# Optimization experiments

Hardware: AMD Instinct MI355X
Metric: run time of the kernel (lower is better)

## Reference

```python
import jax, jax.numpy as jnp
import numpy as np

EPS = 1e-4

def softmax_kernel(data, projection_matrix, is_query):
    # data: [b,h,n,d]; projection_matrix: [m,d]
    d = data.shape[-1]
    m = projection_matrix.shape[0]
    data_normalizer = d ** -0.25
    ratio = m ** -0.5
    # [b,h,n,m]
    data_dash = jnp.einsum('bhnd,md->bhnm', data_normalizer * data, projection_matrix)
    diag_data = jnp.sum(data ** 2, axis=-1, keepdims=True) * 0.5 * data_normalizer ** 2  # [b,h,n,1]
    if is_query:
        stab = jnp.max(data_dash, axis=-1, keepdims=True)
    else:
        stab = jnp.max(data_dash)
    return ratio * (jnp.exp(data_dash - diag_data - stab) + EPS)

def linear_attention(q, k, v):
    # q,k: [b,h,n,m]; v: [b,h,n,e]
    L = k.shape[-2]
    D_inv = 1.0 / jnp.einsum('bhnm,bhm->bhn', q, jnp.mean(k, axis=-2))  # [b,h,n]
    context = jnp.einsum('bhnm,bhne->bhme', k / float(L), v)            # [b,h,m,e]
    out = jnp.einsum('bhnm,bhme->bhne', D_inv[..., None] * q, context)  # [b,h,n,e]
    return out

def setup_inputs() -> dict:
    key = jax.random.key(0)
    k1, k2, k3, k4 = jax.random.split(key, 4)
    b, h, n, d = 4, 8, 4096, 64
    m = 266  # int(d * log(d))
    q = jax.random.normal(k1, (b, h, n, d), dtype=jnp.float32)
    k = jax.random.normal(k2, (b, h, n, d), dtype=jnp.float32)
    v = jax.random.normal(k3, (b, h, n, d), dtype=jnp.float32)
    projection_matrix = jax.random.normal(k4, (m, d), dtype=jnp.float32)
    return {"q": q, "k": k, "v": v, "projection_matrix": projection_matrix}

def reference(q, k, v, projection_matrix):
    qp = softmax_kernel(q, projection_matrix, is_query=True)
    kp = softmax_kernel(k, projection_matrix, is_query=False)
    return linear_attention(qp, kp, v)
```

## Files before the change

kernel.cpp:

```cpp
#include <hip/hip_runtime.h>
#include <cmath>


namespace {
constexpr float NORM       = 0.35355339059327379f;
constexpr float DIAG_SCALE = 0.0625f;
constexpr float EPSV       = 1e-4f;
constexpr float INV_L      = 1.0f / 4096.0f;

constexpr size_t OFF_PT  = 0;
constexpr size_t OFF_U   = OFF_PT + (size_t)64 * 272;
constexpr size_t OFF_u   = OFF_U + (size_t)32 * 272 * 64;
constexpr size_t OFF_SV  = OFF_u + (size_t)32 * 272;
constexpr size_t OFF_SC  = OFF_SV + (size_t)32 * 64;
constexpr size_t OFF_SK  = OFF_SC + (size_t)32 * 64;
constexpr size_t OFF_S   = OFF_SK + 32;
constexpr size_t OFF_CTX = OFF_S + 4;
constexpr size_t WS_FLOATS = OFF_CTX + (size_t)32 * 272 * 68;
}

__device__ __forceinline__ unsigned fenc(float f) {
  unsigned u = __float_as_uint(f);
  return (u & 0x80000000u) ? ~u : (u | 0x80000000u);
}
__device__ __forceinline__ float fdec(unsigned u) {
  return (u & 0x80000000u) ? __uint_as_float(u ^ 0x80000000u) : __uint_as_float(~u);
}

__device__ __forceinline__ void glds4(const float* g, float* l) {
  __builtin_amdgcn_global_load_lds((const __attribute__((address_space(1))) void*)g,
                                   (__attribute__((address_space(3))) void*)l, 4, 0, 0);
}
__device__ __forceinline__ void glds16(const float* g, float* l) {
  __builtin_amdgcn_global_load_lds((const __attribute__((address_space(1))) void*)g,
                                   (__attribute__((address_space(3))) void*)l, 16, 0, 0);
}

__global__ __launch_bounds__(256) void setup_kernel(const float* __restrict__ P,
                                                    float* __restrict__ ws) {
  const int t = threadIdx.x;
  const int elem = blockIdx.x * 256 + t;
  const int td = elem / 272, mm = elem % 272;
  ws[OFF_PT + (size_t)td * 272 + mm] = (mm < 266) ? NORM * P[mm * 64 + td] : 0.0f;
  if (blockIdx.x == 0 && t == 0) ((unsigned*)(ws + OFF_S))[0] = 0x007FFFFFu;
}

#define KQ_ROW(A1R, K4, P0, P1, P2, P3)                                         \
  {                                                                             \
    A1R[0] = fmaf((K4).x, (P0).x, A1R[0]);                                      \
    A1R[1] = fmaf((K4).x, (P0).y, A1R[1]);                                      \
    A1R[2] = fmaf((K4).x, (P0).z, A1R[2]);                                      \
    A1R[3] = fmaf((K4).x, (P0).w, A1R[3]);                                      \
    A1R[0] = fmaf((K4).y, (P1).x, A1R[0]);                                      \
    A1R[1] = fmaf((K4).y, (P1).y, A1R[1]);                                      \
    A1R[2] = fmaf((K4).y, (P1).z, A1R[2]);                                      \
    A1R[3] = fmaf((K4).y, (P1).w, A1R[3]);                                      \
    A1R[0] = fmaf((K4).z, (P2).x, A1R[0]);                                      \
    A1R[1] = fmaf((K4).z, (P2).y, A1R[1]);                                      \
    A1R[2] = fmaf((K4).z, (P2).z, A1R[2]);                                      \
    A1R[3] = fmaf((K4).z, (P2).w, A1R[3]);                                      \
    A1R[0] = fmaf((K4).w, (P3).x, A1R[0]);                                      \
    A1R[1] = fmaf((K4).w, (P3).y, A1R[1]);                                      \
    A1R[2] = fmaf((K4).w, (P3).z, A1R[2]);                                      \
    A1R[3] = fmaf((K4).w, (P3).w, A1R[3]);                                      \
  }

#define QC_ROW(AR, Q4, C0, C1, C2, C3)                                          \
  {                                                                             \
    AR[0] = fmaf((Q4).x, (C0).x, AR[0]);                                        \
    AR[1] = fmaf((Q4).x, (C0).y, AR[1]);                                        \
    AR[2] = fmaf((Q4).x, (C0).z, AR[2]);                                        \
    AR[3] = fmaf((Q4).x, (C0).w, AR[3]);                                        \
    AR[0] = fmaf((Q4).y, (C1).x, AR[0]);                                        \
    AR[1] = fmaf((Q4).y, (C1).y, AR[1]);                                        \
    AR[2] = fmaf((Q4).y, (C1).z, AR[2]);                                        \
    AR[3] = fmaf((Q4).y, (C1).w, AR[3]);                                        \
    AR[0] = fmaf((Q4).z, (C2).x, AR[0]);                                        \
    AR[1] = fmaf((Q4).z, (C2).y, AR[1]);                                        \
    AR[2] = fmaf((Q4).z, (C2).z, AR[2]);                                        \
    AR[3] = fmaf((Q4).z, (C2).w, AR[3]);                                        \
    AR[0] = fmaf((Q4).w, (C3).x, AR[0]);                                        \
    AR[1] = fmaf((Q4).w, (C3).y, AR[1]);                                        \
    AR[2] = fmaf((Q4).w, (C3).z, AR[2]);                                        \
    AR[3] = fmaf((Q4).w, (C3).w, AR[3]);                                        \
  }

__global__ __launch_bounds__(256) void pass_k_fused(const float* __restrict__ kg,
                                                    const float* __restrict__ vg,
                                                    float* __restrict__ ws) {
  __shared__ __align__(16) float pool[12544];
  __shared__ float diagS[64];
  __shared__ float redb[4];

  const int t = threadIdx.x;
  const int mb = blockIdx.x, bh = blockIdx.y, bz = blockIdx.z;
  const int lane = t & 63, wv = t >> 6;

  float* PTs = pool;
  float* kS  = pool + 4096;
  float* vS  = pool + 8448;

  const size_t base = ((size_t)bh * 4096 + (size_t)bz * 1024) * 64;

  if (mb == 4) {
    const int m4 = t & 3, rg1 = t >> 2;
    const int eg = (t >> 2) & 15, rs = t >> 6;

    {
      const int td = t >> 2, m4i = t & 3;
      *(float4*)(PTs + td * 16 + m4i * 4) =
          *(const float4*)(ws + OFF_PT + (size_t)td * 272 + 256 + m4i * 4);
    }

    float acc2[4][4];
#pragma unroll
    for (int i = 0; i < 4; ++i) { acc2[i][0] = acc2[i][1] = acc2[i][2] = acc2[i][3] = 0.f; }
    float uacc[4] = {0, 0, 0, 0};
    float vsum[4] = {0, 0, 0, 0};
    float smax = -INFINITY;

    for (int sc = 0; sc < 16; ++sc) {
      const float* kgp = kg + base + (size_t)sc * 64 * 64;
      const float* vgp = vg + base + (size_t)sc * 64 * 64;
      __syncthreads();
      {
        const int r0 = wv * 16;
#pragma unroll
        for (int r = 0; r < 16; ++r) glds4(kgp + (r0 + r) * 64 + lane, kS + (r0 + r) * 68);
#pragma unroll
        for (int r4 = 0; r4 < 4; ++r4)
          glds16(vgp + (r0 + r4 * 4) * 64 + lane * 4, vS + (r0 + r4 * 4) * 64);
      }
      __syncthreads();
      {
        const int dr = t >> 2, dq = t & 3;
        const float4 s0 = *(const float4*)(kS + dr * 68 + dq * 16);
        const float4 s1 = *(const float4*)(kS + dr * 68 + dq * 16 + 4);
        const float4 s2 = *(const float4*)(kS + dr * 68 + dq * 16 + 8);
        const float4 s3 = *(const float4*)(kS + dr * 68 + dq * 16 + 12);
        float s = s0.x * s0.x;
        s = fmaf(s0.y, s0.y, s); s = fmaf(s0.z, s0.z, s); s = fmaf(s0.w, s0.w, s);
        s = fmaf(s1.x, s1.x, s); s = fmaf(s1.y, s1.y, s); s = fmaf(s1.z, s1.z, s);
        s = fmaf(s1.w, s1.w, s);
        s = fmaf(s2.x, s2.x, s); s = fmaf(s2.y, s2.y, s); s = fmaf(s2.z, s2.z, s);
        s = fmaf(s2.w, s2.w, s);
        s = fmaf(s3.x, s3.x, s); s = fmaf(s3.y, s3.y, s); s = fmaf(s3.z, s3.z, s);
        s = fmaf(s3.w, s3.w, s);
        s += __shfl_xor(s, 1);
        s += __shfl_xor(s, 2);
        if (dq == 0) diagS[dr] = s * DIAG_SCALE;
      }
      __syncthreads();
      float a1[4] = {0, 0, 0, 0};
#pragma unroll
      for (int tb = 0; tb < 16; ++tb) {
        const int td = tb * 4;
        const float4 kv4 = *(const float4*)(kS + rg1 * 68 + td);
        const float4 p0 = *(const float4*)(PTs + (td + 0) * 16 + m4 * 4);
        const float4 p1 = *(const float4*)(PTs + (td + 1) * 16 + m4 * 4);
        const float4 p2 = *(const float4*)(PTs + (td + 2) * 16 + m4 * 4);
        const float4 p3 = *(const float4*)(PTs + (td + 3) * 16 + m4 * 4);
        KQ_ROW(a1, kv4, p0, p1, p2, p3);
      }
      float vals[4];
      {
        const float dg = diagS[rg1];
#pragma unroll
        for (int j = 0; j < 4; ++j) {
          const int m = 256 + m4 * 4 + j;
          float e = 0.f;
          if (m < 266) {
            smax = fmaxf(smax, a1[j]);
            e = __expf(a1[j] - dg);
          }
          vals[j] = e;
        }
      }
      __syncthreads();
      {
        float4 st;
        st.x = vals[0]; st.y = vals[1]; st.z = vals[2]; st.w = vals[3];
        *(float4*)(kS + rg1 * 20 + m4 * 4) = st;
      }
      __syncthreads();
#pragma unroll 2
      for (int nn = 0; nn < 16; ++nn) {
        const int n = rs * 16 + nn;
        const float4 kk4 = *(const float4*)(kS + n * 20 + m4 * 4);
        const float4 vv4 = *(const float4*)(vS + n * 64 + eg * 4);
        const float kk[4] = {kk4.x, kk4.y, kk4.z, kk4.w};
        const float vv[4] = {vv4.x, vv4.y, vv4.z, vv4.w};
#pragma unroll
        for (int i = 0; i < 4; ++i)
#pragma unroll
          for (int j = 0; j < 4; ++j) acc2[i][j] = fmaf(kk[i], vv[j], acc2[i][j]);
        if (eg == 0) {
#pragma unroll
          for (int i = 0; i < 4; ++i) uacc[i] += kk[i];
        }
        if (m4 == 0) {
          vsum[0] += vv[0]; vsum[1] += vv[1]; vsum[2] += vv[2]; vsum[3] += vv[3];
        }
      }
    }
    {
      float* Ub = ws + OFF_U + ((size_t)bh * 272 + 256 + m4 * 4) * 64 + eg * 4;
#pragma unroll
      for (int i = 0; i < 4; ++i)
#pragma unroll
        for (int j = 0; j < 4; ++j) atomicAdd(Ub + (size_t)i * 64 + j, acc2[i][j]);
      if (eg == 0) {
#pragma unroll
        for (int i = 0; i < 4; ++i)
          atomicAdd(ws + OFF_u + (size_t)bh * 272 + 256 + m4 * 4 + i, uacc[i]);
      }
      if (m4 == 0) {
#pragma unroll
        for (int j = 0; j < 4; ++j)
          atomicAdd(ws + OFF_SV + bh * 64 + eg * 4 + j, vsum[j]);
      }
    }
#pragma unroll
    for (int o = 32; o > 0; o >>= 1) smax = fmaxf(smax, __shfl_xor(smax, o));
    if (lane == 0) redb[wv] = smax;
    __syncthreads();
    if (t == 0) {
      const float m = fmaxf(fmaxf(redb[0], redb[1]), fmaxf(redb[2], redb[3]));
      atomicMax((unsigned*)(ws + OFF_S), fenc(m));
    }
    return;
  }

  const int mq = t & 15, rg = t >> 4;
  const int mo = t & 7, eo = (t >> 3) & 7;
  const int rs = t >> 6;

#pragma unroll
  for (int c = 0; c < 4; ++c) {
    const int f4 = c * 256 + t;
    const int td = f4 >> 4, mi = f4 & 15;
    *(float4*)(PTs + td * 64 + mi * 4) =
        *(const float4*)(ws + OFF_PT + (size_t)td * 272 + mb * 64 + mi * 4);
  }

  float acc2[8][8];
#pragma unroll
  for (int i = 0; i < 8; ++i)
#pragma unroll
    for (int j = 0; j < 8; ++j) acc2[i][j] = 0.f;
  float uacc[8] = {0, 0, 0, 0, 0, 0, 0, 0};
  float smax = -INFINITY;

  for (int sc = 0; sc < 16; ++sc) {
    const float* kgp = kg + base + (size_t)sc * 64 * 64;
    const float* vgp = vg + base + (size_t)sc * 64 * 64;
    __syncthreads();
    {
      const int r0 = wv * 16;
#pragma unroll
      for (int r = 0; r < 16; ++r) glds4(kgp + (r0 + r) * 64 + lane, kS + (r0 + r) * 68);
#pragma unroll
      for (int r4 = 0; r4 < 4; ++r4)
        glds16(vgp + (r0 + r4 * 4) * 64 + lane * 4, vS + (r0 + r4 * 4) * 64);
    }
    __syncthreads();
    {
      const int dr = t >> 2, dq = t & 3;
      const float4 s0 = *(const float4*)(kS + dr * 68 + dq * 16);
      const float4 s1 = *(const float4*)(kS + dr * 68 + dq * 16 + 4);
      const float4 s2 = *(const float4*)(kS + dr * 68 + dq * 16 + 8);
      const float4 s3 = *(const float4*)(kS + dr * 68 + dq * 16 + 12);
      float s = s0.x * s0.x;
      s = fmaf(s0.y, s0.y, s); s = fmaf(s0.z, s0.z, s); s = fmaf(s0.w, s0.w, s);
      s = fmaf(s1.x, s1.x, s); s = fmaf(s1.y, s1.y, s); s = fmaf(s1.z, s1.z, s);
      s = fmaf(s1.w, s1.w, s);
      s = fmaf(s2.x, s2.x, s); s = fmaf(s2.y, s2.y, s); s = fmaf(s2.z, s2.z, s);
      s = fmaf(s2.w, s2.w, s);
      s = fmaf(s3.x, s3.x, s); s = fmaf(s3.y, s3.y, s); s = fmaf(s3.z, s3.z, s);
      s = fmaf(s3.w, s3.w, s);
      s += __shfl_xor(s, 1);
      s += __shfl_xor(s, 2);
      if (dq == 0) diagS[dr] = s * DIAG_SCALE;
    }
    __syncthreads();

    float a1[4][4];
#pragma unroll
    for (int i = 0; i < 4; ++i) { a1[i][0] = a1[i][1] = a1[i][2] = a1[i][3] = 0.f; }
#pragma unroll
    for (int tb = 0; tb < 16; ++tb) {
      const int td = tb * 4;
      const float4 kA = *(const float4*)(kS + (rg * 4 + 0) * 68 + td);
      const float4 kB = *(const float4*)(kS + (rg * 4 + 1) * 68 + td);
      const float4 kC = *(const float4*)(kS + (rg * 4 + 2) * 68 + td);
      const float4 kD = *(const float4*)(kS + (rg * 4 + 3) * 68 + td);
      const float4 p0 = *(const float4*)(PTs + (td + 0) * 64 + mq * 4);
      const float4 p1 = *(const float4*)(PTs + (td + 1) * 64 + mq * 4);
      const float4 p2 = *(const float4*)(PTs + (td + 2) * 64 + mq * 4);
      const float4 p3 = *(const float4*)(PTs + (td + 3) * 64 + mq * 4);
      KQ_ROW(a1[0], kA, p0, p1, p2, p3);
      KQ_ROW(a1[1], kB, p0, p1, p2, p3);
      KQ_ROW(a1[2], kC, p0, p1, p2, p3);
      KQ_ROW(a1[3], kD, p0, p1, p2, p3);
    }
#pragma unroll
    for (int i = 0; i < 4; ++i) {
      const float dg = diagS[rg * 4 + i];
      smax = fmaxf(smax, fmaxf(fmaxf(a1[i][0], a1[i][1]), fmaxf(a1[i][2], a1[i][3])));
      a1[i][0] = __expf(a1[i][0] - dg);
      a1[i][1] = __expf(a1[i][1] - dg);
      a1[i][2] = __expf(a1[i][2] - dg);
      a1[i][3] = __expf(a1[i][3] - dg);
    }
    __syncthreads();
#pragma unroll
    for (int i = 0; i < 4; ++i) {
      float4 st;
      st.x = a1[i][0]; st.y = a1[i][1]; st.z = a1[i][2]; st.w = a1[i][3];
      *(float4*)(kS + (rg * 4 + i) * 68 + mq * 4) = st;
    }
    __syncthreads();
#pragma unroll 2
    for (int nn = 0; nn < 16; ++nn) {
      const int n = rs * 16 + nn;
      const float4 ka = *(const float4*)(kS + n * 68 + mo * 8);
      const float4 kb = *(const float4*)(kS + n * 68 + mo * 8 + 4);
      const float4 va = *(const float4*)(vS + n * 64 + eo * 8);
      const float4 vb = *(const float4*)(vS + n * 64 + eo * 8 + 4);
      const float kk[8] = {ka.x, ka.y, ka.z, ka.w, kb.x, kb.y, kb.z, kb.w};
      const float vv[8] = {va.x, va.y, va.z, va.w, vb.x, vb.y, vb.z, vb.w};
#pragma unroll
      for (int i = 0; i < 8; ++i)
#pragma unroll
        for (int j = 0; j < 8; ++j) acc2[i][j] = fmaf(kk[i], vv[j], acc2[i][j]);
      if (eo == 0) {
#pragma unroll
        for (int i = 0; i < 8; ++i) uacc[i] += kk[i];
      }
    }
  }

  __syncthreads();
  {
    float* FA = vS;
    float* FB = PTs;
    if (wv == 1) {
#pragma unroll
      for (int i = 0; i < 8; ++i)
#pragma unroll
        for (int j = 0; j < 8; ++j) FA[(i * 8 + j) * 64 + lane] = acc2[i][j];
    }
    if (wv == 3) {
#pragma unroll
      for (int i = 0; i < 8; ++i)
#pragma unroll
        for (int j = 0; j < 8; ++j) FB[(i * 8 + j) * 64 + lane] = acc2[i][j];
    }
    __syncthreads();
    if (wv == 0) {
#pragma unroll
      for (int i = 0; i < 8; ++i)
#pragma unroll
        for (int j = 0; j < 8; ++j) acc2[i][j] += FA[(i * 8 + j) * 64 + lane];
    }
    if (wv == 2) {
#pragma unroll
      for (int i = 0; i < 8; ++i)
#pragma unroll
        for (int j = 0; j < 8; ++j) acc2[i][j] += FB[(i * 8 + j) * 64 + lane];
    }
    __syncthreads();
    if (wv == 2) {
#pragma unroll
      for (int i = 0; i < 8; ++i)
#pragma unroll
        for (int j = 0; j < 8; ++j) FA[(i * 8 + j) * 64 + lane] = acc2[i][j];
    }
    __syncthreads();
    if (wv == 0) {
      const int mo8 = (lane & 7) * 8, eo8 = (lane >> 3) * 8;
#pragma unroll
      for (int i = 0; i < 8; ++i)
#pragma unroll
        for (int j = 0; j < 8; ++j) {
          acc2[i][j] += FA[(i * 8 + j) * 64 + lane];
          kS[(mo8 + i) * 65 + eo8 + j] = acc2[i][j];
        }
    }
    __syncthreads();
    {
      float* Ub = ws + OFF_U + ((size_t)bh * 272 + mb * 64) * 64;
#pragma unroll
      for (int r = 0; r < 16; ++r) {
        const int row = wv * 16 + r;
        atomicAdd(Ub + (size_t)row * 64 + lane, kS[row * 65 + lane]);
      }
    }
    if (eo == 0) {
#pragma unroll
      for (int i = 0; i < 8; ++i)
        atomicAdd(ws + OFF_u + (size_t)bh * 272 + mb * 64 + mo * 8 + i, uacc[i]);
    }
  }
#pragma unroll
  for (int o = 32; o > 0; o >>= 1) smax = fmaxf(smax, __shfl_xor(smax, o));
  if (lane == 0) redb[wv] = smax;
  __syncthreads();
  if (t == 0) {
    const float m = fmaxf(fmaxf(redb[0], redb[1]), fmaxf(redb[2], redb[3]));
    atomicMax((unsigned*)(ws + OFF_S), fenc(m));
  }
}

__global__ __launch_bounds__(256) void combine_kernel(float* __restrict__ ws) {
  __shared__ float red[256];
  const int t = threadIdx.x;
  const int bh = blockIdx.x;
  const float S = fdec(((unsigned*)(ws + OFF_S))[0]);
  const float es = __expf(-S);
  const int e = t & 63, mr = t >> 6;
  const float svv = ws[OFF_SV + bh * 64 + e];
  float scp = 0.f;
  for (int mm = mr; mm < 272; mm += 4) {
    float val = 0.f;
    if (mm < 266)
      val = (es * ws[OFF_U + ((size_t)bh * 272 + mm) * 64 + e] + EPSV * svv) * INV_L;
    ws[OFF_CTX + ((size_t)bh * 272 + mm) * 68 + e] = val;
    scp += val;
  }
  red[t] = scp;
  __syncthreads();
  if (t < 64) ws[OFF_SC + bh * 64 + t] = red[t] + red[t + 64] + red[t + 128] + red[t + 192];
  __syncthreads();
  float skp = 0.f;
  for (int mm = t; mm < 272; mm += 256) {
    float km = 0.f;
    if (mm < 266) km = es * ws[OFF_u + (size_t)bh * 272 + mm] * INV_L + EPSV;
    float* cx = ws + OFF_CTX + ((size_t)bh * 272 + mm) * 68;
    cx[64] = km; cx[65] = 0.f; cx[66] = 0.f; cx[67] = 0.f;
    skp += km;
  }
  red[t] = skp;
  __syncthreads();
  for (int s = 128; s > 0; s >>= 1) {
    if (t < s) red[t] += red[t + s];
    __syncthreads();
  }
  if (t == 0) ws[OFF_SK + bh] = red[0];
}

__global__ __launch_bounds__(256) void pass_q(const float* __restrict__ qg,
                                              float* __restrict__ outg,
                                              const float* __restrict__ ws) {
  __shared__ __align__(16) float uni[8704];
  __shared__ float diagS[32];
  __shared__ unsigned rmx[32];
  __shared__ float Bl[32];

  const int t = threadIdx.x;
  const int nt = blockIdx.x, bh = blockIdx.y;
  const int lane = t & 63, wv = t >> 6;
  const float* qgp = qg + ((size_t)bh * 4096 + (size_t)nt * 32) * 64;

  if (t < 32) rmx[t] = 0x007FFFFFu;

#pragma unroll
  for (int r = 0; r < 8; ++r)
    glds4(qgp + (wv * 8 + r) * 64 + lane, uni + (wv * 8 + r) * 68);
  {
    const int td = t >> 2, j4 = t & 3;
    *(float4*)(uni + 2176 + td * 16 + j4 * 4) =
        *(const float4*)(ws + OFF_PT + (size_t)td * 272 + 256 + j4 * 4);
  }
  __syncthreads();

  {
    const int dr = t >> 3, d8 = t & 7;
    const float4 s0 = *(const float4*)(uni + dr * 68 + d8 * 8);
    const float4 s1 = *(const float4*)(uni + dr * 68 + d8 * 8 + 4);
    float s = s0.x * s0.x;
    s = fmaf(s0.y, s0.y, s); s = fmaf(s0.z, s0.z, s); s = fmaf(s0.w, s0.w, s);
    s = fmaf(s1.x, s1.x, s); s = fmaf(s1.y, s1.y, s); s = fmaf(s1.z, s1.z, s);
    s = fmaf(s1.w, s1.w, s);
    s += __shfl_xor(s, 1);
    s += __shfl_xor(s, 2);
    s += __shfl_xor(s, 4);
    if (d8 == 0) diagS[dr] = s * DIAG_SCALE;
  }
  __syncthreads();

  const int mq = t & 63;
  float a1[8][4];
#pragma unroll
  for (int i = 0; i < 8; ++i) { a1[i][0] = a1[i][1] = a1[i][2] = a1[i][3] = 0.f; }
  {
    const float* ptm = ws + OFF_PT + mq * 4;
    float4 pfA0, pfA1, pfA2, pfA3, pfB0, pfB1, pfB2, pfB3;
    pfA0 = *(const float4*)(ptm + (size_t)0 * 272);
    pfA1 = *(const float4*)(ptm + (size_t)1 * 272);
    pfA2 = *(const float4*)(ptm + (size_t)2 * 272);
    pfA3 = *(const float4*)(ptm + (size_t)3 * 272);
    pfB0 = *(const float4*)(ptm + (size_t)4 * 272);
    pfB1 = *(const float4*)(ptm + (size_t)5 * 272);
    pfB2 = *(const float4*)(ptm + (size_t)6 * 272);
    pfB3 = *(const float4*)(ptm + (size_t)7 * 272);
#pragma unroll
    for (int tb = 0; tb < 16; tb += 2) {
      {
        const int td = tb * 4;
#pragma unroll
        for (int i = 0; i < 8; ++i) {
          const float4 q4 = *(const float4*)(uni + (wv * 8 + i) * 68 + td);
          KQ_ROW(a1[i], q4, pfA0, pfA1, pfA2, pfA3);
        }
        if (tb < 14) {
          pfA0 = *(const float4*)(ptm + (size_t)(td + 8) * 272);
          pfA1 = *(const float4*)(ptm + (size_t)(td + 9) * 272);
          pfA2 = *(const float4*)(ptm + (size_t)(td + 10) * 272);
          pfA3 = *(const float4*)(ptm + (size_t)(td + 11) * 272);
        }
      }
      {
        const int td = tb * 4 + 4;
#pragma unroll
        for (int i = 0; i < 8; ++i) {
          const float4 q4 = *(const float4*)(uni + (wv * 8 + i) * 68 + td);
          KQ_ROW(a1[i], q4, pfB0, pfB1, pfB2, pfB3);
        }
        if (tb < 14) {
          pfB0 = *(const float4*)(ptm + (size_t)(td + 8) * 272);
          pfB1 = *(const float4*)(ptm + (size_t)(td + 9) * 272);
          pfB2 = *(const float4*)(ptm + (size_t)(td + 10) * 272);
          pfB3 = *(const float4*)(ptm + (size_t)(td + 11) * 272);
        }
      }
    }
  }
  float at[2] = {0.f, 0.f};
  const int mtl = t & 15;
  const int mt = 256 + mtl;
  const int r2 = (t >> 4) * 2;
  {
    const float* pts = uni + 2176 + mtl;
#pragma unroll
    for (int tb = 0; tb < 16; ++tb) {
      const int td = tb * 4;
      const float4 qx4 = *(const float4*)(uni + r2 * 68 + td);
      const float4 qy4 = *(const float4*)(uni + (r2 + 1) * 68 + td);
      const float p0 = pts[(td + 0) * 16];
      const float p1 = pts[(td + 1) * 16];
      const float p2 = pts[(td + 2) * 16];
      const float p3 = pts[(td + 3) * 16];
      at[0] = fmaf(qx4.x, p0, at[0]);
      at[0] = fmaf(qx4.y, p1, at[0]);
      at[0] = fmaf(qx4.z, p2, at[0]);
      at[0] = fmaf(qx4.w, p3, at[0]);
      at[1] = fmaf(qy4.x, p0, at[1]);
      at[1] = fmaf(qy4.y, p1, at[1]);
      at[1] = fmaf(qy4.z, p2, at[1]);
      at[1] = fmaf(qy4.w, p3, at[1]);
    }
  }
  __syncthreads();

#pragma unroll
  for (int i = 0; i < 8; ++i) {
    float lm = fmaxf(fmaxf(a1[i][0], a1[i][1]), fmaxf(a1[i][2], a1[i][3]));
#pragma unroll
    for (int o = 32; o > 0; o >>= 1) lm = fmaxf(lm, __shfl_xor(lm, o));
    if (lane == i) atomicMax(&rmx[wv * 8 + i], fenc(lm));
  }
#pragma unroll
  for (int s = 0; s < 2; ++s) {
    float v = (mt < 266) ? at[s] : -INFINITY;
#pragma unroll
    for (int o = 8; o > 0; o >>= 1) v = fmaxf(v, __shfl_xor(v, o));
    if ((t & 15) == 0) atomicMax(&rmx[r2 + s], fenc(v));
  }
#pragma unroll
  for (int i = 0; i < 8; ++i) {
    const int row = wv * 8 + i;
    const float dg = diagS[row];
    float4 st;
    st.x = __expf(a1[i][0] - dg);
    st.y = __expf(a1[i][1] - dg);
    st.z = __expf(a1[i][2] - dg);
    st.w = __expf(a1[i][3] - dg);
    *(float4*)(uni + row * 272 + mq * 4) = st;
  }
#pragma unroll
  for (int s = 0; s < 2; ++s) {
    const int row = r2 + s;
    uni[row * 272 + mt] = (mt < 266) ? __expf(at[s] - diagS[row]) : 0.f;
  }
  __syncthreads();

  const int cq2 = t & 15, rg2 = (t >> 4) & 7, ms = t >> 7;
  const float* ctxg = ws + OFF_CTX + (size_t)bh * 272 * 68;
  const float* crow = ctxg + cq2 * 4;
  const int mb0 = ms * 136;
  float acc[4][4];
#pragma unroll
  for (int i = 0; i < 4; ++i) { acc[i][0] = acc[i][1] = acc[i][2] = acc[i][3] = 0.f; }
  float accB[4] = {0, 0, 0, 0};
  float4 c0, c1, c2, c3, n0, n1, n2, n3;
  float cb0 = 0, cb1 = 0, cb2 = 0, cb3 = 0, nb0 = 0, nb1 = 0, nb2 = 0, nb3 = 0;
  c0 = *(const float4*)(crow + (size_t)(mb0 + 0) * 68);
  c1 = *(const float4*)(crow + (size_t)(mb0 + 1) * 68);
  c2 = *(const float4*)(crow + (size_t)(mb0 + 2) * 68);
  c3 = *(const float4*)(crow + (size_t)(mb0 + 3) * 68);
  if (cq2 == 0) {
    cb0 = ctxg[(size_t)(mb0 + 0) * 68 + 64];
    cb1 = ctxg[(size_t)(mb0 + 1) * 68 + 64];
    cb2 = ctxg[(size_t)(mb0 + 2) * 68 + 64];
    cb3 = ctxg[(size_t)(mb0 + 3) * 68 + 64];
  }
  for (int mc = 0; mc < 34; ++mc) {
    const int mm = mb0 + mc * 4;
    if (mc < 33) {
      n0 = *(const float4*)(crow + (size_t)(mm + 4) * 68);
      n1 = *(const float4*)(crow + (size_t)(mm + 5) * 68);
      n2 = *(const float4*)(crow + (size_t)(mm + 6) * 68);
      n3 = *(const float4*)(crow + (size_t)(mm + 7) * 68);
      if (cq2 == 0) {
        nb0 = ctxg[(size_t)(mm + 4) * 68 + 64];
        nb1 = ctxg[(size_t)(mm + 5) * 68 + 64];
        nb2 = ctxg[(size_t)(mm + 6) * 68 + 64];
        nb3 = ctxg[(size_t)(mm + 7) * 68 + 64];
      }
    }
    const float4 q0 = *(const float4*)(uni + (rg2 * 4 + 0) * 272 + mm);
    const float4 q1 = *(const float4*)(uni + (rg2 * 4 + 1) * 272 + mm);
    const float4 q2 = *(const float4*)(uni + (rg2 * 4 + 2) * 272 + mm);
    const float4 q3 = *(const float4*)(uni + (rg2 * 4 + 3) * 272 + mm);
    QC_ROW(acc[0], q0, c0, c1, c2, c3);
    QC_ROW(acc[1], q1, c0, c1, c2, c3);
    QC_ROW(acc[2], q2, c0, c1, c2, c3);
    QC_ROW(acc[3], q3, c0, c1, c2, c3);
    if (cq2 == 0) {
      accB[0] = fmaf(q0.x, cb0, accB[0]);
      accB[0] = fmaf(q0.y, cb1, accB[0]);
      accB[0] = fmaf(q0.z, cb2, accB[0]);
      accB[0] = fmaf(q0.w, cb3, accB[0]);
      accB[1] = fmaf(q1.x, cb0, accB[1]);
      accB[1] = fmaf(q1.y, cb1, accB[1]);
      accB[1] = fmaf(q1.z, cb2, accB[1]);
      accB[1] = fmaf(q1.w, cb3, accB[1]);
      accB[2] = fmaf(q2.x, cb0, accB[2]);
      accB[2] = fmaf(q2.y, cb1, accB[2]);
      accB[2] = fmaf(q2.z, cb2, accB[2]);
      accB[2] = fmaf(q2.w, cb3, accB[2]);
      accB[3] = fmaf(q3.x, cb0, accB[3]);
      accB[3] = fmaf(q3.y, cb1, accB[3]);
      accB[3] = fmaf(q3.z, cb2, accB[3]);
      accB[3] = fmaf(q3.w, cb3, accB[3]);
    }
    if (mc < 33) {
      c0 = n0; c1 = n1; c2 = n2; c3 = n3;
      cb0 = nb0; cb1 = nb1; cb2 = nb2; cb3 = nb3;
    }
  }

  __syncthreads();
  if (ms == 1) {
    const int p = t - 128;
#pragma unroll
    for (int i = 0; i < 4; ++i)
#pragma unroll
      for (int j = 0; j < 4; ++j) uni[(i * 4 + j) * 128 + p] = acc[i][j];
    if (cq2 == 0) {
#pragma unroll
      for (int i = 0; i < 4; ++i) uni[2048 + rg2 * 4 + i] = accB[i];
    }
  }
  __syncthreads();
  if (ms == 0) {
#pragma unroll
    for (int i = 0; i < 4; ++i)
#pragma unroll
      for (int j = 0; j < 4; ++j) acc[i][j] += uni[(i * 4 + j) * 128 + t];
    if (cq2 == 0) {
#pragma unroll
      for (int i = 0; i < 4; ++i) Bl[rg2 * 4 + i] = accB[i] + uni[2048 + rg2 * 4 + i];
    }
  }
  __syncthreads();

  if (ms == 0) {
    const float4 sc4 = *(const float4*)(ws + OFF_SC + bh * 64 + cq2 * 4);
    const float skv = ws[OFF_SK + bh];
    float* op = outg + ((size_t)bh * 4096 + (size_t)nt * 32) * 64;
#pragma unroll
    for (int i = 0; i < 4; ++i) {
      const int row = rg2 * 4 + i;
      const float rm = fdec(rmx[row]);
      const float tt = EPSV * __expf(rm);
      const float inv = 1.0f / (Bl[row] + tt * skv);
      float4 o;
      o.x = (acc[i][0] + tt * sc4.x) * inv;
      o.y = (acc[i][1] + tt * sc4.y) * inv;
      o.z = (acc[i][2] + tt * sc4.z) * inv;
      o.w = (acc[i][3] + tt * sc4.w) * inv;
      *(float4*)(op + row * 64 + cq2 * 4) = o;
    }
  }
}

extern "C" void kernel_launch(void* const* d_in, const int* in_sizes, int n_in,
                              void* d_out, int out_size, void* d_ws, size_t ws_size,
                              hipStream_t stream) {
  (void)in_sizes; (void)n_in; (void)out_size; (void)ws_size;
  const float* q = (const float*)d_in[0];
  const float* k = (const float*)d_in[1];
  const float* v = (const float*)d_in[2];
  const float* P = (const float*)d_in[3];
  float* out = (float*)d_out;
  float* ws = (float*)d_ws;

  hipMemsetAsync((void*)(ws + OFF_U), 0, (OFF_CTX - OFF_U) * sizeof(float), stream);
  setup_kernel<<<68, 256, 0, stream>>>(P, ws);
  pass_k_fused<<<dim3(5, 32, 4), 256, 0, stream>>>(k, v, ws);
  combine_kernel<<<32, 256, 0, stream>>>(ws);
  pass_q<<<dim3(128, 32), 256, 0, stream>>>(q, out, ws);
}
```

Baseline: 488.3 us.

## Double-buffer K/V tiles with async prefetch in main pass_k_fused path

Splits the shared-memory K tile into separate raw-K (X) and exp-K (Y) buffers and issues the global-to-LDS loads for the next chunk's K and V before the current chunk's compute finishes. This overlaps global memory latency with the projection and outer-product math. Full __syncthreads calls are replaced with explicit s_waitcnt vmcnt/lgkmcnt plus raw s_barrier. The final reduction scratch layout is also changed. The cost is more LDS per block, which may reduce occupancy, and a wrapped extra prefetch on the last iteration.

```diff
diff --git a/kernel.cpp b/kernel.cpp
--- a/kernel.cpp
+++ b/kernel.cpp
@@ -88,7 +88,7 @@
 __global__ __launch_bounds__(256) void pass_k_fused(const float* __restrict__ kg,
                                                     const float* __restrict__ vg,
                                                     float* __restrict__ ws) {
-  __shared__ __align__(16) float pool[12544];
+  __shared__ __align__(16) float pool[16896];
   __shared__ float diagS[64];
   __shared__ float redb[4];
 
@@ -97,12 +97,15 @@
   const int lane = t & 63, wv = t >> 6;
 
   float* PTs = pool;
-  float* kS  = pool + 4096;
-  float* vS  = pool + 8448;
+  float* X   = pool + 4096;
+  float* Y   = pool + 8448;
+  float* vS  = pool + 12800;
 
   const size_t base = ((size_t)bh * 4096 + (size_t)bz * 1024) * 64;
 
   if (mb == 4) {
+    float* kS  = X;
+    float* vSt = Y;
     const int m4 = t & 3, rg1 = t >> 2;
     const int eg = (t >> 2) & 15, rs = t >> 6;
 
@@ -129,7 +132,7 @@
         for (int r = 0; r < 16; ++r) glds4(kgp + (r0 + r) * 64 + lane, kS + (r0 + r) * 68);
 #pragma unroll
         for (int r4 = 0; r4 < 4; ++r4)
-          glds16(vgp + (r0 + r4 * 4) * 64 + lane * 4, vS + (r0 + r4 * 4) * 64);
+          glds16(vgp + (r0 + r4 * 4) * 64 + lane * 4, vSt + (r0 + r4 * 4) * 64);
       }
       __syncthreads();
       {
@@ -187,7 +190,7 @@
       for (int nn = 0; nn < 16; ++nn) {
         const int n = rs * 16 + nn;
         const float4 kk4 = *(const float4*)(kS + n * 20 + m4 * 4);
-        const float4 vv4 = *(const float4*)(vS + n * 64 + eg * 4);
+        const float4 vv4 = *(const float4*)(vSt + n * 64 + eg * 4);
         const float kk[4] = {kk4.x, kk4.y, kk4.z, kk4.w};
         const float vv[4] = {vv4.x, vv4.y, vv4.z, vv4.w};
 #pragma unroll
@@ -234,6 +237,7 @@
   const int mq = t & 15, rg = t >> 4;
   const int mo = t & 7, eo = (t >> 3) & 7;
   const int rs = t >> 6;
+  const int r0 = wv * 16;
 
 #pragma unroll
   for (int c = 0; c < 4; ++c) {
@@ -242,6 +246,15 @@
     *(float4*)(PTs + td * 64 + mi * 4) =
         *(const float4*)(ws + OFF_PT + (size_t)td * 272 + mb * 64 + mi * 4);
   }
+  {
+    const float* kgp = kg + base;
+    const float* vgp = vg + base;
+#pragma unroll
+    for (int r = 0; r < 16; ++r) glds4(kgp + (r0 + r) * 64 + lane, X + (r0 + r) * 68);
+#pragma unroll
+    for (int r4 = 0; r4 < 4; ++r4)
+      glds16(vgp + (r0 + r4 * 4) * 64 + lane * 4, vS + (r0 + r4 * 4) * 64);
+  }
 
   float acc2[8][8];
 #pragma unroll
@@ -252,24 +265,15 @@
   float smax = -INFINITY;
 
   for (int sc = 0; sc < 16; ++sc) {
-    const float* kgp = kg + base + (size_t)sc * 64 * 64;
-    const float* vgp = vg + base + (size_t)sc * 64 * 64;
-    __syncthreads();
-    {
-      const int r0 = wv * 16;
-#pragma unroll
-      for (int r = 0; r < 16; ++r) glds4(kgp + (r0 + r) * 64 + lane, kS + (r0 + r) * 68);
-#pragma unroll
-      for (int r4 = 0; r4 < 4; ++r4)
-        glds16(vgp + (r0 + r4 * 4) * 64 + lane * 4, vS + (r0 + r4 * 4) * 64);
-    }
-    __syncthreads();
+    asm volatile("s_waitcnt vmcnt(4) lgkmcnt(0)" ::: "memory");
+    __builtin_amdgcn_s_barrier();
+
     {
       const int dr = t >> 2, dq = t & 3;
-      const float4 s0 = *(const float4*)(kS + dr * 68 + dq * 16);
-      const float4 s1 = *(const float4*)(kS + dr * 68 + dq * 16 + 4);
-      const float4 s2 = *(const float4*)(kS + dr * 68 + dq * 16 + 8);
-      const float4 s3 = *(const float4*)(kS + dr * 68 + dq * 16 + 12);
+      const float4 s0 = *(const float4*)(X + dr * 68 + dq * 16);
+      const float4 s1 = *(const float4*)(X + dr * 68 + dq * 16 + 4);
+      const float4 s2 = *(const float4*)(X + dr * 68 + dq * 16 + 8);
+      const float4 s3 = *(const float4*)(X + dr * 68 + dq * 16 + 12);
       float s = s0.x * s0.x;
       s = fmaf(s0.y, s0.y, s); s = fmaf(s0.z, s0.z, s); s = fmaf(s0.w, s0.w, s);
       s = fmaf(s1.x, s1.x, s); s = fmaf(s1.y, s1.y, s); s = fmaf(s1.z, s1.z, s);
@@ -282,7 +286,8 @@
       s += __shfl_xor(s, 2);
       if (dq == 0) diagS[dr] = s * DIAG_SCALE;
     }
-    __syncthreads();
+    asm volatile("s_waitcnt lgkmcnt(0)" ::: "memory");
+    __builtin_amdgcn_s_barrier();
 
     float a1[4][4];
 #pragma unroll
@@ -290,10 +295,10 @@
 #pragma unroll
     for (int tb = 0; tb < 16; ++tb) {
       const int td = tb * 4;
-      const float4 kA = *(const float4*)(kS + (rg * 4 + 0) * 68 + td);
-      const float4 kB = *(const float4*)(kS + (rg * 4 + 1) * 68 + td);
-      const float4 kC = *(const float4*)(kS + (rg * 4 + 2) * 68 + td);
-      const float4 kD = *(const float4*)(kS + (rg * 4 + 3) * 68 + td);
+      const float4 kA = *(const float4*)(X + (rg * 4 + 0) * 68 + td);
+      const float4 kB = *(const float4*)(X + (rg * 4 + 1) * 68 + td);
+      const float4 kC = *(const float4*)(X + (rg * 4 + 2) * 68 + td);
+      const float4 kD = *(const float4*)(X + (rg * 4 + 3) * 68 + td);
       const float4 p0 = *(const float4*)(PTs + (td + 0) * 64 + mq * 4);
       const float4 p1 = *(const float4*)(PTs + (td + 1) * 64 + mq * 4);
       const float4 p2 = *(const float4*)(PTs + (td + 2) * 64 + mq * 4);
@@ -312,19 +317,29 @@
       a1[i][2] = __expf(a1[i][2] - dg);
       a1[i][3] = __expf(a1[i][3] - dg);
     }
-    __syncthreads();
+    asm volatile("s_waitcnt lgkmcnt(0)" ::: "memory");
+    __builtin_amdgcn_s_barrier();
+
+    {
+      const int scn = (sc + 1) & 15;
+      const float* kgp = kg + base + (size_t)scn * 64 * 64;
+#pragma unroll
+      for (int r = 0; r < 16; ++r) glds4(kgp + (r0 + r) * 64 + lane, X + (r0 + r) * 68);
+    }
 #pragma unroll
     for (int i = 0; i < 4; ++i) {
       float4 st;
       st.x = a1[i][0]; st.y = a1[i][1]; st.z = a1[i][2]; st.w = a1[i][3];
-      *(float4*)(kS + (rg * 4 + i) * 68 + mq * 4) = st;
-    }
-    __syncthreads();
+      *(float4*)(Y + (rg * 4 + i) * 68 + mq * 4) = st;
+    }
+    asm volatile("s_waitcnt vmcnt(16) lgkmcnt(0)" ::: "memory");
+    __builtin_amdgcn_s_barrier();
+
 #pragma unroll 2
     for (int nn = 0; nn < 16; ++nn) {
       const int n = rs * 16 + nn;
-      const float4 ka = *(const float4*)(kS + n * 68 + mo * 8);
-      const float4 kb = *(const float4*)(kS + n * 68 + mo * 8 + 4);
+      const float4 ka = *(const float4*)(Y + n * 68 + mo * 8);
+      const float4 kb = *(const float4*)(Y + n * 68 + mo * 8 + 4);
       const float4 va = *(const float4*)(vS + n * 64 + eo * 8);
       const float4 vb = *(const float4*)(vS + n * 64 + eo * 8 + 4);
       const float kk[8] = {ka.x, ka.y, ka.z, ka.w, kb.x, kb.y, kb.z, kb.w};
@@ -338,11 +353,21 @@
         for (int i = 0; i < 8; ++i) uacc[i] += kk[i];
       }
     }
+    asm volatile("s_waitcnt lgkmcnt(0)" ::: "memory");
+    __builtin_amdgcn_s_barrier();
+
+    {
+      const int scn = (sc + 1) & 15;
+      const float* vgp = vg + base + (size_t)scn * 64 * 64;
+#pragma unroll
+      for (int r4 = 0; r4 < 4; ++r4)
+        glds16(vgp + (r0 + r4 * 4) * 64 + lane * 4, vS + (r0 + r4 * 4) * 64);
+    }
   }
 
   __syncthreads();
   {
-    float* FA = vS;
+    float* FA = Y;
     float* FB = PTs;
     if (wv == 1) {
 #pragma unroll
@@ -378,13 +403,12 @@
     }
     __syncthreads();
     if (wv == 0) {
-      const int mo8 = (lane & 7) * 8, eo8 = (lane >> 3) * 8;
 #pragma unroll
       for (int i = 0; i < 8; ++i)
 #pragma unroll
         for (int j = 0; j < 8; ++j) {
           acc2[i][j] += FA[(i * 8 + j) * 64 + lane];
-          kS[(mo8 + i) * 65 + eo8 + j] = acc2[i][j];
+          X[lane * 65 + i * 8 + j] = acc2[i][j];
         }
     }
     __syncthreads();
@@ -393,7 +417,9 @@
 #pragma unroll
       for (int r = 0; r < 16; ++r) {
         const int row = wv * 16 + r;
-        atomicAdd(Ub + (size_t)row * 64 + lane, kS[row * 65 + lane]);
+        const int lp = (row >> 3) + 8 * (lane >> 3);
+        const int idx = (row & 7) * 8 + (lane & 7);
+        atomicAdd(Ub + (size_t)row * 64 + lane, X[lp * 65 + idx]);
       }
     }
     if (eo == 0) {
```

Measured after the change: 499.1 us. +2.2%, slower.
